# Kernel tuning notes

Measured on AMD Instinct MI355X. Metric: run time of the kernel, lower is better.

The kernel has to match this reference:

```python
import jax, jax.numpy as jnp
import numpy as np

N, E, NFEAT, H = 100000, 1600000, 128, 128
NLAYER = 3


def setup_inputs() -> dict:
    key = jax.random.key(0)
    ks = jax.random.split(key, 20)
    s = 0.05
    return {
        "features": jax.random.normal(ks[0], (N, NFEAT), jnp.float32),
        "edge_index": jax.random.randint(ks[1], (2, E), 0, N, jnp.int32),
        "edge_weight": jax.random.uniform(ks[2], (E,), jnp.float32),
        "w1": jax.random.normal(ks[3], (H, NFEAT), jnp.float32) * s,
        "b1": jnp.zeros((H,), jnp.float32),
        "gin_w1": jax.random.normal(ks[4], (NLAYER, H, H), jnp.float32) * s,
        "gin_b1": jnp.zeros((NLAYER, H), jnp.float32),
        "gin_w2": jax.random.normal(ks[5], (NLAYER, H, H), jnp.float32) * s,
        "gin_b2": jnp.zeros((NLAYER, H), jnp.float32),
        "gru_wih": jax.random.normal(ks[6], (NLAYER, 3 * H, H), jnp.float32) * s,
        "gru_whh": jax.random.normal(ks[7], (NLAYER, 3 * H, H), jnp.float32) * s,
        "gru_bih": jnp.zeros((NLAYER, 3 * H), jnp.float32),
        "gru_bhh": jnp.zeros((NLAYER, 3 * H), jnp.float32),
        "head_w1": jax.random.normal(ks[8], (NLAYER, H, H), jnp.float32) * s,
        "head_b1": jnp.zeros((NLAYER, H), jnp.float32),
        "head_w2_0": jax.random.normal(ks[9], (2, H), jnp.float32) * s,
        "head_b2_0": jnp.zeros((2,), jnp.float32),
        "head_w2_1": jax.random.normal(ks[10], (6, H), jnp.float32) * s,
        "head_b2_1": jnp.zeros((6,), jnp.float32),
        "head_w2_2": jax.random.normal(ks[11], (21, H), jnp.float32) * s,
        "head_b2_2": jnp.zeros((21,), jnp.float32),
    }


def _gru_cell(x, h, wih, whh, bih, bhh):
    # torch.nn.GRUCell semantics
    gi = x @ wih.T + bih           # [N, 3H]
    gh = h @ whh.T + bhh           # [N, 3H]
    ir, iz, inn = jnp.split(gi, 3, axis=1)
    hr, hz, hn = jnp.split(gh, 3, axis=1)
    r = jax.nn.sigmoid(ir + hr)
    z = jax.nn.sigmoid(iz + hz)
    n = jnp.tanh(inn + r * hn)
    return (1.0 - z) * n + z * h


def reference(features, edge_index, edge_weight, w1, b1,
              gin_w1, gin_b1, gin_w2, gin_b2,
              gru_wih, gru_whh, gru_bih, gru_bhh,
              head_w1, head_b1,
              head_w2_0, head_b2_0, head_w2_1, head_b2_1, head_w2_2, head_b2_2):
    n_nodes = features.shape[0]
    dst, src = edge_index[0], edge_index[1]  # spmm: out[dst] += w * x[src]
    head_w2 = [head_w2_0, head_w2_1, head_w2_2]
    head_b2 = [head_b2_0, head_b2_1, head_b2_2]

    x = jax.nn.relu(features @ w1.T + b1)  # mlp1 + ReLU
    layer_info = x
    outputs, _outputs = [], []
    for i in range(NLAYER):
        agg = jax.ops.segment_sum(edge_weight[:, None] * x[src], dst,
                                  num_segments=n_nodes)
        h = _gru_cell(agg, layer_info, gru_wih[i], gru_whh[i],
                      gru_bih[i], gru_bhh[i])
        # GinMlp: Linear -> ReLU -> Linear, then outer ReLU
        x = jax.nn.relu(h @ gin_w1[i].T + gin_b1[i]) @ gin_w2[i].T + gin_b2[i]
        x = jax.nn.relu(x)
        # custom layer-norm variant
        x = x / jnp.sqrt(1.0 + jnp.sum(x * x, axis=1, keepdims=True))
        # prediction head for this layer (mlpPos = [0,1,2])
        tmp = jax.nn.relu(x @ head_w1[i].T + head_b1[i]) @ head_w2[i].T + head_b2[i]
        outputs.append(jax.nn.log_softmax(tmp, axis=1))
        _outputs.append(jax.nn.softmax(tmp, axis=1))
        layer_info = x
    return tuple(outputs) + tuple(_outputs)
```

## Files before the change

### kernel.cpp

```cpp
#include <hip/hip_runtime.h>
#include <cstdint>
#include <cstddef>


typedef short  v8s __attribute__((ext_vector_type(8)));
typedef float  v4f __attribute__((ext_vector_type(4)));

#define BUCKET_CAP 4096

static __device__ __forceinline__ float bf2f(uint16_t u) {
  return __uint_as_float(((uint32_t)u) << 16);
}
static __device__ __forceinline__ uint16_t f2b(float f) {
  uint32_t x = __float_as_uint(f);
  return (uint16_t)((x + 0x7FFFu + ((x >> 16) & 1u)) >> 16);
}
static __device__ __forceinline__ float sigmoidf_(float v) {
  return 1.f / (1.f + __expf(-v));
}
static __device__ __forceinline__ float tanhf_(float v) {
  return 1.f - 2.f / (__expf(2.f * v) + 1.f);
}

__global__ void k_detect(const uint32_t* __restrict__ u, int* __restrict__ flag) {
  int lane = threadIdx.x;
  uint32_t low = u[lane] & 0xFFFFu;
  uint32_t e = (low >> 7) & 0xFFu;
  bool pass = (e == 0) || (e >= 110 && e <= 141);
  unsigned long long b = __ballot(pass);
  if (lane == 0) *flag = (__popcll(b) >= 32) ? 1 : 0;
}

struct CvtDesc {
  const void* src[18];
  int off[19];
};

__global__ void k_cvtw(CvtDesc c, float* __restrict__ wbase,
                       uint16_t* __restrict__ wb16,
                       const int* __restrict__ flag, int total) {
  int gid = blockIdx.x * 256 + threadIdx.x;
  if (gid >= total) return;
  int t = 0;
#pragma unroll
  for (int i = 1; i < 18; i++)
    if (gid >= c.off[i]) t = i;
  int local = gid - c.off[t];
  float v;
  if (*flag) v = bf2f(((const uint16_t*)c.src[t])[local]);
  else       v = ((const float*)c.src[t])[local];
  wbase[gid] = v;
  wb16[gid] = f2b(v);
}

__global__ void k_cvt_feat(const void* __restrict__ src, uint16_t* __restrict__ dst,
                           int n, const int* __restrict__ flag) {
  int i = blockIdx.x * 256 + threadIdx.x;
  if (i >= n) return;
  if (*flag) dst[i] = ((const uint16_t*)src)[i];
  else       dst[i] = f2b(((const float*)src)[i]);
}

__global__ void k_zero_i(int* __restrict__ p, int n) {
  int i = blockIdx.x * 256 + threadIdx.x;
  if (i < n) p[i] = 0;
}

__global__ void k_zero_f(float* __restrict__ p, int n) {
  int i = blockIdx.x * 256 + threadIdx.x;
  if (i < n) p[i] = 0.f;
}

__global__ void k_pack_mm(const uint16_t* __restrict__ src, uint16_t* __restrict__ dst,
                          int nmat) {
  int id = blockIdx.x * 256 + threadIdx.x;
  if (id >= nmat * 2048) return;
  int mat = id >> 11;
  int rem = id & 2047;
  int blk = rem >> 6, lane = rem & 63;
  int kc = blk >> 3, t = blk & 7;
  int n0 = lane & 15, quad = lane >> 4;
  const uint16_t* s = src + (size_t)mat * 16384 + (size_t)(t * 16 + n0) * 128 + kc * 32 + quad * 8;
  uint16_t* d = dst + (size_t)id * 8;
  *reinterpret_cast<v8s*>(d) = *reinterpret_cast<const v8s*>(s);
}

__global__ void k_pack_gru(const uint16_t* __restrict__ wih, const uint16_t* __restrict__ whh,
                           uint16_t* __restrict__ dst, int nlayer) {
  int id = blockIdx.x * 256 + threadIdx.x;
  if (id >= nlayer * 192 * 64) return;
  int lane = id & 63;
  int blk = (id >> 6) % 192;
  int layer = (id >> 6) / 192;
  int g = blk % 3;
  int mat = (blk / 3) % 2;
  int u = (blk / 6) % 2;
  int w = (blk / 12) % 4;
  int kc = blk / 48;
  int n0 = lane & 15, quad = lane >> 4;
  const uint16_t* base = (mat == 0 ? wih : whh) + (size_t)layer * 384 * 128;
  const uint16_t* s = base + (size_t)(g * 128 + w * 32 + u * 16 + n0) * 128 + kc * 32 + quad * 8;
  uint16_t* d = dst + ((size_t)layer * 192 + blk) * 512 + (size_t)lane * 8;
  *reinterpret_cast<v8s*>(d) = *reinterpret_cast<const v8s*>(s);
}

__global__ void k_part(const int* __restrict__ dst, const int* __restrict__ src,
                       const void* __restrict__ w, int* __restrict__ gcur,
                       uint2* __restrict__ ep0, const int* __restrict__ flag,
                       int E, int NB) {
  __shared__ int hist[1024];
  __shared__ int lbase[1024];
  int t = threadIdx.x;
  int CH = (E + gridDim.x - 1) / gridDim.x;
  int e0 = blockIdx.x * CH;
  int e1 = e0 + CH;
  if (e1 > E) e1 = E;
  for (int b = t; b < NB; b += 256) hist[b] = 0;
  __syncthreads();
  for (int e = e0 + t; e < e1; e += 256)
    atomicAdd(&hist[dst[e] >> 7], 1);
  __syncthreads();
  for (int b = t; b < NB; b += 256) {
    int c = hist[b];
    lbase[b] = c ? atomicAdd(&gcur[b], c) : 0;
    hist[b] = 0;
  }
  __syncthreads();
  bool bf = (*flag) != 0;
  for (int e = e0 + t; e < e1; e += 256) {
    int d = dst[e];
    int b = d >> 7;
    int pos = lbase[b] + atomicAdd(&hist[b], 1);
    if (pos >= BUCKET_CAP) pos = BUCKET_CAP - 1;
    float wv = bf ? bf2f(((const uint16_t*)w)[e]) : ((const float*)w)[e];
    ep0[(size_t)b * BUCKET_CAP + pos] =
        make_uint2((uint32_t)src[e] | (((uint32_t)d & 127u) << 25),
                   __float_as_uint(wv));
  }
}

__global__ void k_bprefix(const int* __restrict__ gcur, int* __restrict__ bbase,
                          int nbuckets) {
  __shared__ int red[256];
  int t = threadIdx.x;
  int chunk = (nbuckets + 255) >> 8;
  int beg = t * chunk;
  int end = beg + chunk;
  if (end > nbuckets) end = nbuckets;
  int s = 0;
  for (int b = beg; b < end; b++) {
    int c = gcur[b];
    if (c > BUCKET_CAP) c = BUCKET_CAP;
    bbase[b] = c;
    s += c;
  }
  red[t] = s;
  __syncthreads();
  for (int off = 1; off < 256; off <<= 1) {
    int u = (t >= off) ? red[t - off] : 0;
    __syncthreads();
    red[t] += u;
    __syncthreads();
  }
  int run = red[t] - s;
  for (int b = beg; b < end; b++) {
    int tot = bbase[b];
    bbase[b] = run;
    run += tot;
  }
}

__global__ void k_build(const uint2* __restrict__ ep0, const int* __restrict__ gcur,
                        const int* __restrict__ bbase, int* __restrict__ rowptr,
                        uint2* __restrict__ ep, int n, int nbuckets) {
  __shared__ int lcnt[128];
  __shared__ int lsc[128];
  int b = blockIdx.x, t = threadIdx.x;
  int cnt = gcur[b];
  if (cnt > BUCKET_CAP) cnt = BUCKET_CAP;
  if (t < 128) lcnt[t] = 0;
  __syncthreads();

  const uint2* sp = ep0 + (size_t)b * BUCKET_CAP;
  for (int p = t; p < cnt; p += 256)
    atomicAdd(&lcnt[sp[p].x >> 25], 1);
  __syncthreads();

  if (t < 128) lsc[t] = lcnt[t];
  __syncthreads();
  for (int off = 1; off < 128; off <<= 1) {
    int v = 0;
    if (t < 128 && t >= off) v = lsc[t - off];
    __syncthreads();
    if (t < 128) lsc[t] += v;
    __syncthreads();
  }

  int base = bbase[b];
  if (t < 128) {
    int excl = lsc[t] - lcnt[t];
    int node = b * 128 + t;
    if (node < n) rowptr[node] = base + excl;
    lcnt[t] = base + excl;
  }
  if (b == nbuckets - 1 && t == 0) rowptr[n] = base + lsc[127];
  __syncthreads();

  for (int p = t; p < cnt; p += 256) {
    uint2 v = sp[p];
    int pos = atomicAdd(&lcnt[v.x >> 25], 1);
    ep[pos] = make_uint2(v.x & 0x01FFFFFFu, v.y);
  }
}

__global__ void k_spmm(const uint16_t* __restrict__ x, const int* __restrict__ rowptr,
                       const uint2* __restrict__ ep, uint16_t* __restrict__ agg, int n) {
  int node = blockIdx.x * 4 + (threadIdx.x >> 6);
  int lane = threadIdx.x & 63;
  if (node >= n) return;
  int p0 = rowptr[node], p1 = rowptr[node + 1];
  float a0 = 0.f, a1 = 0.f;
  const uint16_t* xc = x + (size_t)lane * 2;
  int p = p0;
  for (; p + 7 < p1; p += 8) {
    uint2 e0 = ep[p], e1 = ep[p + 1], e2 = ep[p + 2], e3 = ep[p + 3];
    uint2 e4 = ep[p + 4], e5 = ep[p + 5], e6 = ep[p + 6], e7 = ep[p + 7];
    uint32_t u0 = *reinterpret_cast<const uint32_t*>(xc + (size_t)e0.x * 128);
    uint32_t u1 = *reinterpret_cast<const uint32_t*>(xc + (size_t)e1.x * 128);
    uint32_t u2 = *reinterpret_cast<const uint32_t*>(xc + (size_t)e2.x * 128);
    uint32_t u3 = *reinterpret_cast<const uint32_t*>(xc + (size_t)e3.x * 128);
    uint32_t u4 = *reinterpret_cast<const uint32_t*>(xc + (size_t)e4.x * 128);
    uint32_t u5 = *reinterpret_cast<const uint32_t*>(xc + (size_t)e5.x * 128);
    uint32_t u6 = *reinterpret_cast<const uint32_t*>(xc + (size_t)e6.x * 128);
    uint32_t u7 = *reinterpret_cast<const uint32_t*>(xc + (size_t)e7.x * 128);
    float w0 = __uint_as_float(e0.y), w1 = __uint_as_float(e1.y);
    float w2 = __uint_as_float(e2.y), w3 = __uint_as_float(e3.y);
    float w4 = __uint_as_float(e4.y), w5 = __uint_as_float(e5.y);
    float w6 = __uint_as_float(e6.y), w7 = __uint_as_float(e7.y);
    a0 = fmaf(w0, bf2f((uint16_t)u0), a0);
    a1 = fmaf(w0, bf2f((uint16_t)(u0 >> 16)), a1);
    a0 = fmaf(w1, bf2f((uint16_t)u1), a0);
    a1 = fmaf(w1, bf2f((uint16_t)(u1 >> 16)), a1);
    a0 = fmaf(w2, bf2f((uint16_t)u2), a0);
    a1 = fmaf(w2, bf2f((uint16_t)(u2 >> 16)), a1);
    a0 = fmaf(w3, bf2f((uint16_t)u3), a0);
    a1 = fmaf(w3, bf2f((uint16_t)(u3 >> 16)), a1);
    a0 = fmaf(w4, bf2f((uint16_t)u4), a0);
    a1 = fmaf(w4, bf2f((uint16_t)(u4 >> 16)), a1);
    a0 = fmaf(w5, bf2f((uint16_t)u5), a0);
    a1 = fmaf(w5, bf2f((uint16_t)(u5 >> 16)), a1);
    a0 = fmaf(w6, bf2f((uint16_t)u6), a0);
    a1 = fmaf(w6, bf2f((uint16_t)(u6 >> 16)), a1);
    a0 = fmaf(w7, bf2f((uint16_t)u7), a0);
    a1 = fmaf(w7, bf2f((uint16_t)(u7 >> 16)), a1);
  }
  for (; p + 1 < p1; p += 2) {
    uint2 e0 = ep[p], e1 = ep[p + 1];
    uint32_t u0 = *reinterpret_cast<const uint32_t*>(xc + (size_t)e0.x * 128);
    uint32_t u1 = *reinterpret_cast<const uint32_t*>(xc + (size_t)e1.x * 128);
    float w0 = __uint_as_float(e0.y), w1 = __uint_as_float(e1.y);
    a0 = fmaf(w0, bf2f((uint16_t)u0), a0);
    a1 = fmaf(w0, bf2f((uint16_t)(u0 >> 16)), a1);
    a0 = fmaf(w1, bf2f((uint16_t)u1), a0);
    a1 = fmaf(w1, bf2f((uint16_t)(u1 >> 16)), a1);
  }
  for (; p < p1; p++) {
    uint2 e0 = ep[p];
    float w0 = __uint_as_float(e0.y);
    uint32_t u0 = *reinterpret_cast<const uint32_t*>(xc + (size_t)e0.x * 128);
    a0 = fmaf(w0, bf2f((uint16_t)u0), a0);
    a1 = fmaf(w0, bf2f((uint16_t)(u0 >> 16)), a1);
  }
  uint32_t packed = (uint32_t)f2b(a0) | ((uint32_t)f2b(a1) << 16);
  *reinterpret_cast<uint32_t*>(agg + (size_t)node * 128 + lane * 2) = packed;
}

template <int EPI>
__launch_bounds__(256)
__global__ void k_mm(const uint16_t* __restrict__ A, const uint16_t* __restrict__ Wrp,
                     const float* __restrict__ bias, uint16_t* __restrict__ C,
                     int nrows) {
  int wave = threadIdx.x >> 6, lane = threadIdx.x & 63;
  int n0 = lane & 15, quad = lane >> 4;
  int m0 = (blockIdx.x * 4 + wave) * 32;
  int r0 = m0 + n0, r1 = m0 + 16 + n0;
  bool ok0 = r0 < nrows, ok1 = r1 < nrows;
  const v8s z8 = {0, 0, 0, 0, 0, 0, 0, 0};

  v4f acc[2][8];
#pragma unroll
  for (int rt = 0; rt < 2; rt++)
#pragma unroll
    for (int t = 0; t < 8; t++) acc[rt][t] = {0.f, 0.f, 0.f, 0.f};

  const uint16_t* ap0 = A + (size_t)r0 * 128 + quad * 8;
  const uint16_t* ap1 = A + (size_t)r1 * 128 + quad * 8;
#pragma unroll
  for (int kc = 0; kc < 4; kc++) {
    v8s a0 = ok0 ? *reinterpret_cast<const v8s*>(ap0 + kc * 32) : z8;
    v8s a1 = ok1 ? *reinterpret_cast<const v8s*>(ap1 + kc * 32) : z8;
    const uint16_t* wp = Wrp + (size_t)kc * 4096 + (size_t)lane * 8;
#pragma unroll
    for (int t = 0; t < 8; t++) {
      v8s bf = *reinterpret_cast<const v8s*>(wp + t * 512);
      acc[0][t] = __builtin_amdgcn_mfma_f32_16x16x32_bf16(a0, bf, acc[0][t], 0, 0, 0);
      acc[1][t] = __builtin_amdgcn_mfma_f32_16x16x32_bf16(a1, bf, acc[1][t], 0, 0, 0);
    }
  }

#pragma unroll
  for (int rt = 0; rt < 2; rt++) {
    int mb = m0 + rt * 16;
    float vv[8][4];
#pragma unroll
    for (int t = 0; t < 8; t++) {
      float b = bias[t * 16 + n0];
#pragma unroll
      for (int r = 0; r < 4; r++) vv[t][r] = fmaxf(acc[rt][t][r] + b, 0.f);
    }
    if (EPI == 2) {
#pragma unroll
      for (int r = 0; r < 4; r++) {
        float ss = 0.f;
#pragma unroll
        for (int t = 0; t < 8; t++) ss = fmaf(vv[t][r], vv[t][r], ss);
        ss += __shfl_xor(ss, 1);
        ss += __shfl_xor(ss, 2);
        ss += __shfl_xor(ss, 4);
        ss += __shfl_xor(ss, 8);
        float sc = rsqrtf(1.f + ss);
#pragma unroll
        for (int t = 0; t < 8; t++) vv[t][r] *= sc;
      }
    }
#pragma unroll
    for (int r = 0; r < 4; r++) {
      int row = mb + quad * 4 + r;
      if (row >= nrows) continue;
#pragma unroll
      for (int t = 0; t < 8; t++)
        C[(size_t)row * 128 + t * 16 + n0] = f2b(vv[t][r]);
    }
  }
}

template <int C>
__launch_bounds__(256)
__global__ void k_mm12h(const uint16_t* __restrict__ A,
                        const uint16_t* __restrict__ W1rp, const float* __restrict__ b1,
                        const uint16_t* __restrict__ W2rp, const float* __restrict__ b2,
                        const uint16_t* __restrict__ Whrp, const float* __restrict__ bh,
                        const float* __restrict__ w2, const float* __restrict__ b2h,
                        uint16_t* __restrict__ xbout,
                        float* __restrict__ out_log, float* __restrict__ out_soft,
                        int nrows) {
  __shared__ uint16_t hl[128][136];
  int wave = threadIdx.x >> 6, lane = threadIdx.x & 63;
  int n0 = lane & 15, quad = lane >> 4;
  int m0 = (blockIdx.x * 4 + wave) * 32;
  int r0 = m0 + n0, r1 = m0 + 16 + n0;
  bool ok0 = r0 < nrows, ok1 = r1 < nrows;
  const v8s z8 = {0, 0, 0, 0, 0, 0, 0, 0};

  v4f acc[2][8];
#pragma unroll
  for (int rt = 0; rt < 2; rt++)
#pragma unroll
    for (int t = 0; t < 8; t++) acc[rt][t] = {0.f, 0.f, 0.f, 0.f};

  const uint16_t* ap0 = A + (size_t)r0 * 128 + quad * 8;
  const uint16_t* ap1 = A + (size_t)r1 * 128 + quad * 8;
#pragma unroll
  for (int kc = 0; kc < 4; kc++) {
    v8s a0 = ok0 ? *reinterpret_cast<const v8s*>(ap0 + kc * 32) : z8;
    v8s a1 = ok1 ? *reinterpret_cast<const v8s*>(ap1 + kc * 32) : z8;
    const uint16_t* wp = W1rp + (size_t)kc * 4096 + (size_t)lane * 8;
#pragma unroll
    for (int t = 0; t < 8; t++) {
      v8s bf = *reinterpret_cast<const v8s*>(wp + t * 512);
      acc[0][t] = __builtin_amdgcn_mfma_f32_16x16x32_bf16(a0, bf, acc[0][t], 0, 0, 0);
      acc[1][t] = __builtin_amdgcn_mfma_f32_16x16x32_bf16(a1, bf, acc[1][t], 0, 0, 0);
    }
  }
#pragma unroll
  for (int rt = 0; rt < 2; rt++) {
#pragma unroll
    for (int t = 0; t < 8; t++) {
      float b = b1[t * 16 + n0];
#pragma unroll
      for (int r = 0; r < 4; r++) {
        int rl = wave * 32 + rt * 16 + quad * 4 + r;
        hl[rl][t * 16 + n0] = f2b(fmaxf(acc[rt][t][r] + b, 0.f));
      }
    }
  }
  __syncthreads();

  v4f acc2[2][8];
#pragma unroll
  for (int rt = 0; rt < 2; rt++)
#pragma unroll
    for (int t = 0; t < 8; t++) acc2[rt][t] = {0.f, 0.f, 0.f, 0.f};
#pragma unroll
  for (int kc = 0; kc < 4; kc++) {
    v8s a0 = *reinterpret_cast<const v8s*>(&hl[wave * 32 + n0][kc * 32 + quad * 8]);
    v8s a1 = *reinterpret_cast<const v8s*>(&hl[wave * 32 + 16 + n0][kc * 32 + quad * 8]);
    const uint16_t* wp = W2rp + (size_t)kc * 4096 + (size_t)lane * 8;
#pragma unroll
    for (int t = 0; t < 8; t++) {
      v8s bf = *reinterpret_cast<const v8s*>(wp + t * 512);
      acc2[0][t] = __builtin_amdgcn_mfma_f32_16x16x32_bf16(a0, bf, acc2[0][t], 0, 0, 0);
      acc2[1][t] = __builtin_amdgcn_mfma_f32_16x16x32_bf16(a1, bf, acc2[1][t], 0, 0, 0);
    }
  }
  __syncthreads();
#pragma unroll
  for (int rt = 0; rt < 2; rt++) {
    int mb = m0 + rt * 16;
    float vv[8][4];
#pragma unroll
    for (int t = 0; t < 8; t++) {
      float b = b2[t * 16 + n0];
#pragma unroll
      for (int r = 0; r < 4; r++) vv[t][r] = fmaxf(acc2[rt][t][r] + b, 0.f);
    }
#pragma unroll
    for (int r = 0; r < 4; r++) {
      float ss = 0.f;
#pragma unroll
      for (int t = 0; t < 8; t++) ss = fmaf(vv[t][r], vv[t][r], ss);
      ss += __shfl_xor(ss, 1);
      ss += __shfl_xor(ss, 2);
      ss += __shfl_xor(ss, 4);
      ss += __shfl_xor(ss, 8);
      float sc = rsqrtf(1.f + ss);
#pragma unroll
      for (int t = 0; t < 8; t++) vv[t][r] *= sc;
    }
#pragma unroll
    for (int r = 0; r < 4; r++) {
      int row = mb + quad * 4 + r;
      int rl = wave * 32 + rt * 16 + quad * 4 + r;
#pragma unroll
      for (int t = 0; t < 8; t++) {
        uint16_t hv = f2b(vv[t][r]);
        hl[rl][t * 16 + n0] = hv;
        if (row < nrows) xbout[(size_t)row * 128 + t * 16 + n0] = hv;
      }
    }
  }
  __syncthreads();

  v4f acc3[2][8];
#pragma unroll
  for (int rt = 0; rt < 2; rt++)
#pragma unroll
    for (int t = 0; t < 8; t++) acc3[rt][t] = {0.f, 0.f, 0.f, 0.f};
#pragma unroll
  for (int kc = 0; kc < 4; kc++) {
    v8s a0 = *reinterpret_cast<const v8s*>(&hl[wave * 32 + n0][kc * 32 + quad * 8]);
    v8s a1 = *reinterpret_cast<const v8s*>(&hl[wave * 32 + 16 + n0][kc * 32 + quad * 8]);
    const uint16_t* wp = Whrp + (size_t)kc * 4096 + (size_t)lane * 8;
#pragma unroll
    for (int t = 0; t < 8; t++) {
      v8s bf = *reinterpret_cast<const v8s*>(wp + t * 512);
      acc3[0][t] = __builtin_amdgcn_mfma_f32_16x16x32_bf16(a0, bf, acc3[0][t], 0, 0, 0);
      acc3[1][t] = __builtin_amdgcn_mfma_f32_16x16x32_bf16(a1, bf, acc3[1][t], 0, 0, 0);
    }
  }
  __syncthreads();
#pragma unroll
  for (int rt = 0; rt < 2; rt++) {
#pragma unroll
    for (int t = 0; t < 8; t++) {
      float b = bh[t * 16 + n0];
#pragma unroll
      for (int r = 0; r < 4; r++) {
        int rl = wave * 32 + rt * 16 + quad * 4 + r;
        hl[rl][t * 16 + n0] = f2b(fmaxf(acc3[rt][t][r] + b, 0.f));
      }
    }
  }
  __syncthreads();

  int tid = threadIdx.x;
  if (tid < 128) {
    int node = blockIdx.x * 128 + tid;
    if (node < nrows) {
      float lg[C];
#pragma unroll
      for (int c = 0; c < C; c++) lg[c] = b2h[c];
      for (int k = 0; k < 64; k++) {
        uint32_t u = *reinterpret_cast<const uint32_t*>(&hl[tid][2 * k]);
        float x0 = bf2f((uint16_t)u);
        float x1 = bf2f((uint16_t)(u >> 16));
#pragma unroll
        for (int c = 0; c < C; c++) lg[c] = fmaf(x0, w2[c * 128 + 2 * k], lg[c]);
#pragma unroll
        for (int c = 0; c < C; c++) lg[c] = fmaf(x1, w2[c * 128 + 2 * k + 1], lg[c]);
      }
      float m = lg[0];
#pragma unroll
      for (int c = 1; c < C; c++) m = fmaxf(m, lg[c]);
      float sum = 0.f;
      float e[C];
#pragma unroll
      for (int c = 0; c < C; c++) { e[c] = __expf(lg[c] - m); sum += e[c]; }
      float ls = __logf(sum);
      float inv = 1.f / sum;
#pragma unroll
      for (int c = 0; c < C; c++) {
        out_log[(size_t)node * C + c] = lg[c] - m - ls;
        out_soft[(size_t)node * C + c] = e[c] * inv;
      }
    }
  }
}

__launch_bounds__(512, 2)
__global__ void k_gru8(const uint16_t* __restrict__ agg, const uint16_t* __restrict__ xb,
                       const uint16_t* __restrict__ Wrp,
                       const float* __restrict__ bih, const float* __restrict__ bhh,
                       uint16_t* __restrict__ hb, int n, int ntiles) {
  int wave = threadIdx.x >> 6, lane = threadIdx.x & 63;
  int n0 = lane & 15, quad = lane >> 4;
  int s = wave >> 1, u = wave & 1;
  const v8s z8 = {0, 0, 0, 0, 0, 0, 0, 0};

  v8s wf[24];
#pragma unroll
  for (int kc = 0; kc < 4; kc++)
#pragma unroll
    for (int mat = 0; mat < 2; mat++)
#pragma unroll
      for (int g = 0; g < 3; g++)
        wf[kc * 6 + mat * 3 + g] = *reinterpret_cast<const v8s*>(
            Wrp + (size_t)((kc * 4 + s) * 12 + (u * 2 + mat) * 3 + g) * 512 +
            (size_t)lane * 8);

  int col = wave * 16 + n0;
  float bir = bih[col], biz = bih[128 + col], bin = bih[256 + col];
  float bhr = bhh[col], bhz = bhh[128 + col], bhn = bhh[256 + col];

  for (int tt = blockIdx.x; tt < ntiles; tt += gridDim.x) {
    int m0 = tt * 32;
    int r0 = m0 + n0, r1 = m0 + 16 + n0;
    bool ok0 = r0 < n, ok1 = r1 < n;

    v4f accI[2][3], accH[2][3];
#pragma unroll
    for (int rt = 0; rt < 2; rt++)
#pragma unroll
      for (int g = 0; g < 3; g++) {
        accI[rt][g] = {0.f, 0.f, 0.f, 0.f};
        accH[rt][g] = {0.f, 0.f, 0.f, 0.f};
      }

    const uint16_t* ap0 = agg + (size_t)r0 * 128 + quad * 8;
    const uint16_t* ap1 = agg + (size_t)r1 * 128 + quad * 8;
    const uint16_t* xp0 = xb + (size_t)r0 * 128 + quad * 8;
    const uint16_t* xp1 = xb + (size_t)r1 * 128 + quad * 8;
#pragma unroll
    for (int kc = 0; kc < 4; kc++) {
      v8s a0 = ok0 ? *reinterpret_cast<const v8s*>(ap0 + kc * 32) : z8;
      v8s a1 = ok1 ? *reinterpret_cast<const v8s*>(ap1 + kc * 32) : z8;
      v8s x0 = ok0 ? *reinterpret_cast<const v8s*>(xp0 + kc * 32) : z8;
      v8s x1 = ok1 ? *reinterpret_cast<const v8s*>(xp1 + kc * 32) : z8;
#pragma unroll
      for (int g = 0; g < 3; g++) {
        accI[0][g] = __builtin_amdgcn_mfma_f32_16x16x32_bf16(a0, wf[kc * 6 + g], accI[0][g], 0, 0, 0);
        accI[1][g] = __builtin_amdgcn_mfma_f32_16x16x32_bf16(a1, wf[kc * 6 + g], accI[1][g], 0, 0, 0);
        accH[0][g] = __builtin_amdgcn_mfma_f32_16x16x32_bf16(x0, wf[kc * 6 + 3 + g], accH[0][g], 0, 0, 0);
        accH[1][g] = __builtin_amdgcn_mfma_f32_16x16x32_bf16(x1, wf[kc * 6 + 3 + g], accH[1][g], 0, 0, 0);
      }
    }

#pragma unroll
    for (int rt = 0; rt < 2; rt++) {
#pragma unroll
      for (int r = 0; r < 4; r++) {
        int row = m0 + rt * 16 + quad * 4 + r;
        if (row < n) {
          float ir = accI[rt][0][r] + bir;
          float iz = accI[rt][1][r] + biz;
          float in_ = accI[rt][2][r] + bin;
          float hr = accH[rt][0][r] + bhr;
          float hz = accH[rt][1][r] + bhz;
          float hn = accH[rt][2][r] + bhn;
          float rr = sigmoidf_(ir + hr);
          float zz = sigmoidf_(iz + hz);
          float nn = tanhf_(fmaf(rr, hn, in_));
          float xv = bf2f(xb[(size_t)row * 128 + col]);
          hb[(size_t)row * 128 + col] = f2b(fmaf(zz, xv - nn, nn));
        }
      }
    }
  }
}

extern "C" void kernel_launch(void* const* d_in, const int* in_sizes, int n_in,
                              void* d_out, int out_size, void* d_ws, size_t ws_size,
                              hipStream_t stream) {
  const int N = in_sizes[0] / 128;
  const int E = in_sizes[2];
  const int NB = (N + 127) >> 7;

  static const int wn[18] = {16384, 128, 49152, 384, 49152, 384,
                             147456, 147456, 1152, 1152, 49152, 384,
                             256, 2, 768, 6, 2688, 21};
  CvtDesc cd;
  int off = 0;
  for (int i = 0; i < 18; i++) {
    cd.src[i] = d_in[3 + i];
    cd.off[i] = off;
    off += wn[i];
  }
  cd.off[18] = off;
  const int wtotal = off;

  char* p = (char*)d_ws;
  size_t used = 0;
  auto alloc = [&](size_t bytes) -> char* {
    char* r = p;
    size_t b = (bytes + 255) & ~(size_t)255;
    p += b;
    used += b;
    return r;
  };
  int*      flag    = (int*)alloc(256);
  float*    wbase   = (float*)alloc((size_t)wtotal * 4);
  uint16_t* wb16    = (uint16_t*)alloc((size_t)wtotal * 2);
  uint16_t* mmrp    = (uint16_t*)alloc((size_t)10 * 16384 * 2);
  uint16_t* grurp   = (uint16_t*)alloc((size_t)3 * 192 * 512 * 2);
  uint16_t* xb      = (uint16_t*)alloc((size_t)N * 128 * 2);
  uint16_t* aggb    = (uint16_t*)alloc((size_t)N * 128 * 2);
  uint16_t* hb      = (uint16_t*)alloc((size_t)N * 128 * 2);
  int*      rowptr  = (int*)alloc((size_t)(N + 1) * 4);
  int*      gcur    = (int*)alloc((size_t)NB * 4);
  int*      bbase   = (int*)alloc((size_t)(NB + 1) * 4);
  uint2*    ep0     = (uint2*)alloc((size_t)NB * BUCKET_CAP * 8);
  uint2*    epack   = (uint2*)alloc((size_t)E * 8);

  float* out = (float*)d_out;
  float* outlog[3]  = {out, out + 2 * (size_t)N, out + 8 * (size_t)N};
  float* outsoft[3] = {out + 29 * (size_t)N, out + 31 * (size_t)N, out + 37 * (size_t)N};

  if (used > ws_size) {
    k_zero_f<<<(out_size + 255) / 256, 256, 0, stream>>>(out, out_size);
    return;
  }

  float* b1f   = wbase + cd.off[1];
  float* ginb1 = wbase + cd.off[3];
  float* ginb2 = wbase + cd.off[5];
  float* bih   = wbase + cd.off[8];
  float* bhh   = wbase + cd.off[9];
  float* hb1   = wbase + cd.off[11];
  float* hw2_0 = wbase + cd.off[12];
  float* hb2_0 = wbase + cd.off[13];
  float* hw2_1 = wbase + cd.off[14];
  float* hb2_1 = wbase + cd.off[15];
  float* hw2_2 = wbase + cd.off[16];
  float* hb2_2 = wbase + cd.off[17];

  uint16_t* w1b   = wb16 + cd.off[0];
  uint16_t* ginw1b= wb16 + cd.off[2];
  uint16_t* ginw2b= wb16 + cd.off[4];
  uint16_t* wihb  = wb16 + cd.off[6];
  uint16_t* whhb  = wb16 + cd.off[7];
  uint16_t* hw1b  = wb16 + cd.off[10];

  uint16_t* w1rp    = mmrp;
  uint16_t* ginw1rp = mmrp + (size_t)1 * 16384;
  uint16_t* ginw2rp = mmrp + (size_t)4 * 16384;
  uint16_t* hw1rp   = mmrp + (size_t)7 * 16384;

  const int* dst = (const int*)d_in[1];
  const int* src = (const int*)d_in[1] + E;

  k_detect<<<1, 64, 0, stream>>>((const uint32_t*)d_in[0], flag);
  k_cvtw<<<(wtotal + 255) / 256, 256, 0, stream>>>(cd, wbase, wb16, flag, wtotal);
  k_cvt_feat<<<((size_t)N * 128 + 255) / 256, 256, 0, stream>>>(d_in[0], aggb,
                                                                N * 128, flag);
  k_pack_mm<<<(1 * 2048 + 255) / 256, 256, 0, stream>>>(w1b, w1rp, 1);
  k_pack_mm<<<(3 * 2048 + 255) / 256, 256, 0, stream>>>(ginw1b, ginw1rp, 3);
  k_pack_mm<<<(3 * 2048 + 255) / 256, 256, 0, stream>>>(ginw2b, ginw2rp, 3);
  k_pack_mm<<<(3 * 2048 + 255) / 256, 256, 0, stream>>>(hw1b, hw1rp, 3);
  k_pack_gru<<<(3 * 192 * 64 + 255) / 256, 256, 0, stream>>>(wihb, whhb, grurp, 3);

  k_zero_i<<<(NB + 255) / 256, 256, 0, stream>>>(gcur, NB);
  k_part<<<256, 256, 0, stream>>>(dst, src, d_in[2], gcur, ep0, flag, E, NB);
  k_bprefix<<<1, 256, 0, stream>>>(gcur, bbase, NB);
  k_build<<<NB, 256, 0, stream>>>(ep0, gcur, bbase, rowptr, epack, N, NB);

  int mmrb = (N + 127) / 128;
  int spb  = (N + 3) / 4;
  int ntiles32 = (N + 31) / 32;

  k_mm<1><<<mmrb, 256, 0, stream>>>(aggb, w1rp, b1f, xb, N);

  for (int i = 0; i < 3; i++) {
    k_spmm<<<spb, 256, 0, stream>>>(xb, rowptr, epack, aggb, N);
    k_gru8<<<256, 512, 0, stream>>>(aggb, xb, grurp + (size_t)i * 192 * 512,
                                    bih + i * 384, bhh + i * 384, hb, N, ntiles32);
    if (i == 0)
      k_mm12h<2><<<mmrb, 256, 0, stream>>>(hb, ginw1rp + (size_t)i * 16384,
                                           ginb1 + i * 128,
                                           ginw2rp + (size_t)i * 16384,
                                           ginb2 + i * 128,
                                           hw1rp + (size_t)i * 16384, hb1 + i * 128,
                                           hw2_0, hb2_0, xb,
                                           outlog[0], outsoft[0], N);
    else if (i == 1)
      k_mm12h<6><<<mmrb, 256, 0, stream>>>(hb, ginw1rp + (size_t)i * 16384,
                                           ginb1 + i * 128,
                                           ginw2rp + (size_t)i * 16384,
                                           ginb2 + i * 128,
                                           hw1rp + (size_t)i * 16384, hb1 + i * 128,
                                           hw2_1, hb2_1, xb,
                                           outlog[1], outsoft[1], N);
    else
      k_mm12h<21><<<mmrb, 256, 0, stream>>>(hb, ginw1rp + (size_t)i * 16384,
                                            ginb1 + i * 128,
                                            ginw2rp + (size_t)i * 16384,
                                            ginb2 + i * 128,
                                            hw1rp + (size_t)i * 16384, hb1 + i * 128,
                                            hw2_2, hb2_2, xb,
                                            outlog[2], outsoft[2], N);
  }
}
```

Before: 814.0 us.

## Halve mm12h row tile and split head output across four threads per row

The fused GIN-MLP/head kernel now handles 64 rows per block (16 per wave) instead of 128, which halves the LDS tile and accumulator registers and doubles the block count. The final small head projection changes from 128 threads each doing a full 128-long dot product to all 256 threads, four per row, each covering a quarter of K and combined with xor shuffles. This is meant to raise occupancy and remove the serial tail where half the block sat idle. In exchange, each weight fragment is reused across fewer rows, so weight loads per row double.

Result: slower. 869.2 us (+6.8%).

```diff
diff --git a/kernel.cpp b/kernel.cpp
--- a/kernel.cpp
+++ b/kernel.cpp
@@ -354,75 +354,61 @@
                         uint16_t* __restrict__ xbout,
                         float* __restrict__ out_log, float* __restrict__ out_soft,
                         int nrows) {
-  __shared__ uint16_t hl[128][136];
+  __shared__ uint16_t hl[64][136];
   int wave = threadIdx.x >> 6, lane = threadIdx.x & 63;
   int n0 = lane & 15, quad = lane >> 4;
-  int m0 = (blockIdx.x * 4 + wave) * 32;
-  int r0 = m0 + n0, r1 = m0 + 16 + n0;
-  bool ok0 = r0 < nrows, ok1 = r1 < nrows;
+  int m0 = blockIdx.x * 64 + wave * 16;
+  int r0 = m0 + n0;
+  bool ok0 = r0 < nrows;
   const v8s z8 = {0, 0, 0, 0, 0, 0, 0, 0};
 
-  v4f acc[2][8];
-#pragma unroll
-  for (int rt = 0; rt < 2; rt++)
-#pragma unroll
-    for (int t = 0; t < 8; t++) acc[rt][t] = {0.f, 0.f, 0.f, 0.f};
+  v4f acc[8];
+#pragma unroll
+  for (int t = 0; t < 8; t++) acc[t] = {0.f, 0.f, 0.f, 0.f};
 
   const uint16_t* ap0 = A + (size_t)r0 * 128 + quad * 8;
-  const uint16_t* ap1 = A + (size_t)r1 * 128 + quad * 8;
 #pragma unroll
   for (int kc = 0; kc < 4; kc++) {
     v8s a0 = ok0 ? *reinterpret_cast<const v8s*>(ap0 + kc * 32) : z8;
-    v8s a1 = ok1 ? *reinterpret_cast<const v8s*>(ap1 + kc * 32) : z8;
     const uint16_t* wp = W1rp + (size_t)kc * 4096 + (size_t)lane * 8;
 #pragma unroll
     for (int t = 0; t < 8; t++) {
       v8s bf = *reinterpret_cast<const v8s*>(wp + t * 512);
-      acc[0][t] = __builtin_amdgcn_mfma_f32_16x16x32_bf16(a0, bf, acc[0][t], 0, 0, 0);
-      acc[1][t] = __builtin_amdgcn_mfma_f32_16x16x32_bf16(a1, bf, acc[1][t], 0, 0, 0);
-    }
-  }
-#pragma unroll
-  for (int rt = 0; rt < 2; rt++) {
-#pragma unroll
-    for (int t = 0; t < 8; t++) {
-      float b = b1[t * 16 + n0];
-#pragma unroll
-      for (int r = 0; r < 4; r++) {
-        int rl = wave * 32 + rt * 16 + quad * 4 + r;
-        hl[rl][t * 16 + n0] = f2b(fmaxf(acc[rt][t][r] + b, 0.f));
-      }
-    }
-  }
-  __syncthreads();
-
-  v4f acc2[2][8];
-#pragma unroll
-  for (int rt = 0; rt < 2; rt++)
-#pragma unroll
-    for (int t = 0; t < 8; t++) acc2[rt][t] = {0.f, 0.f, 0.f, 0.f};
+      acc[t] = __builtin_amdgcn_mfma_f32_16x16x32_bf16(a0, bf, acc[t], 0, 0, 0);
+    }
+  }
+#pragma unroll
+  for (int t = 0; t < 8; t++) {
+    float b = b1[t * 16 + n0];
+#pragma unroll
+    for (int r = 0; r < 4; r++) {
+      int rl = wave * 16 + quad * 4 + r;
+      hl[rl][t * 16 + n0] = f2b(fmaxf(acc[t][r] + b, 0.f));
+    }
+  }
+  __syncthreads();
+
+  v4f acc2[8];
+#pragma unroll
+  for (int t = 0; t < 8; t++) acc2[t] = {0.f, 0.f, 0.f, 0.f};
 #pragma unroll
   for (int kc = 0; kc < 4; kc++) {
-    v8s a0 = *reinterpret_cast<const v8s*>(&hl[wave * 32 + n0][kc * 32 + quad * 8]);
-    v8s a1 = *reinterpret_cast<const v8s*>(&hl[wave * 32 + 16 + n0][kc * 32 + quad * 8]);
+    v8s a0 = *reinterpret_cast<const v8s*>(&hl[wave * 16 + n0][kc * 32 + quad * 8]);
     const uint16_t* wp = W2rp + (size_t)kc * 4096 + (size_t)lane * 8;
 #pragma unroll
     for (int t = 0; t < 8; t++) {
       v8s bf = *reinterpret_cast<const v8s*>(wp + t * 512);
-      acc2[0][t] = __builtin_amdgcn_mfma_f32_16x16x32_bf16(a0, bf, acc2[0][t], 0, 0, 0);
-      acc2[1][t] = __builtin_amdgcn_mfma_f32_16x16x32_bf16(a1, bf, acc2[1][t], 0, 0, 0);
-    }
-  }
-  __syncthreads();
-#pragma unroll
-  for (int rt = 0; rt < 2; rt++) {
-    int mb = m0 + rt * 16;
+      acc2[t] = __builtin_amdgcn_mfma_f32_16x16x32_bf16(a0, bf, acc2[t], 0, 0, 0);
+    }
+  }
+  __syncthreads();
+  {
     float vv[8][4];
 #pragma unroll
     for (int t = 0; t < 8; t++) {
       float b = b2[t * 16 + n0];
 #pragma unroll
-      for (int r = 0; r < 4; r++) vv[t][r] = fmaxf(acc2[rt][t][r] + b, 0.f);
+      for (int r = 0; r < 4; r++) vv[t][r] = fmaxf(acc2[t][r] + b, 0.f);
     }
 #pragma unroll
     for (int r = 0; r < 4; r++) {
@@ -439,8 +425,8 @@
     }
 #pragma unroll
     for (int r = 0; r < 4; r++) {
-      int row = mb + quad * 4 + r;
-      int rl = wave * 32 + rt * 16 + quad * 4 + r;
+      int row = m0 + quad * 4 + r;
+      int rl = wave * 16 + quad * 4 + r;
 #pragma unroll
       for (int t = 0; t < 8; t++) {
         uint16_t hv = f2b(vv[t][r]);
@@ -451,54 +437,58 @@
   }
   __syncthreads();
 
-  v4f acc3[2][8];
-#pragma unroll
-  for (int rt = 0; rt < 2; rt++)
-#pragma unroll
-    for (int t = 0; t < 8; t++) acc3[rt][t] = {0.f, 0.f, 0.f, 0.f};
+  v4f acc3[8];
+#pragma unroll
+  for (int t = 0; t < 8; t++) acc3[t] = {0.f, 0.f, 0.f, 0.f};
 #pragma unroll
   for (int kc = 0; kc < 4; kc++) {
-    v8s a0 = *reinterpret_cast<const v8s*>(&hl[wave * 32 + n0][kc * 32 + quad * 8]);
-    v8s a1 = *reinterpret_cast<const v8s*>(&hl[wave * 32 + 16 + n0][kc * 32 + quad * 8]);
+    v8s a0 = *reinterpret_cast<const v8s*>(&hl[wave * 16 + n0][kc * 32 + quad * 8]);
     const uint16_t* wp = Whrp + (size_t)kc * 4096 + (size_t)lane * 8;
 #pragma unroll
     for (int t = 0; t < 8; t++) {
       v8s bf = *reinterpret_cast<const v8s*>(wp + t * 512);
-      acc3[0][t] = __builtin_amdgcn_mfma_f32_16x16x32_bf16(a0, bf, acc3[0][t], 0, 0, 0);
-      acc3[1][t] = __builtin_amdgcn_mfma_f32_16x16x32_bf16(a1, bf, acc3[1][t], 0, 0, 0);
-    }
-  }
-  __syncthreads();
-#pragma unroll
-  for (int rt = 0; rt < 2; rt++) {
-#pragma unroll
-    for (int t = 0; t < 8; t++) {
-      float b = bh[t * 16 + n0];
-#pragma unroll
-      for (int r = 0; r < 4; r++) {
-        int rl = wave * 32 + rt * 16 + quad * 4 + r;
-        hl[rl][t * 16 + n0] = f2b(fmaxf(acc3[rt][t][r] + b, 0.f));
-      }
-    }
-  }
-  __syncthreads();
-
-  int tid = threadIdx.x;
-  if (tid < 128) {
-    int node = blockIdx.x * 128 + tid;
-    if (node < nrows) {
-      float lg[C];
-#pragma unroll
-      for (int c = 0; c < C; c++) lg[c] = b2h[c];
-      for (int k = 0; k < 64; k++) {
-        uint32_t u = *reinterpret_cast<const uint32_t*>(&hl[tid][2 * k]);
-        float x0 = bf2f((uint16_t)u);
-        float x1 = bf2f((uint16_t)(u >> 16));
-#pragma unroll
-        for (int c = 0; c < C; c++) lg[c] = fmaf(x0, w2[c * 128 + 2 * k], lg[c]);
-#pragma unroll
-        for (int c = 0; c < C; c++) lg[c] = fmaf(x1, w2[c * 128 + 2 * k + 1], lg[c]);
-      }
+      acc3[t] = __builtin_amdgcn_mfma_f32_16x16x32_bf16(a0, bf, acc3[t], 0, 0, 0);
+    }
+  }
+  __syncthreads();
+#pragma unroll
+  for (int t = 0; t < 8; t++) {
+    float b = bh[t * 16 + n0];
+#pragma unroll
+    for (int r = 0; r < 4; r++) {
+      int rl = wave * 16 + quad * 4 + r;
+      hl[rl][t * 16 + n0] = f2b(fmaxf(acc3[t][r] + b, 0.f));
+    }
+  }
+  __syncthreads();
+
+  {
+    int row = threadIdx.x >> 2;
+    int s = threadIdx.x & 3;
+    int node = blockIdx.x * 64 + row;
+    float lg[C];
+#pragma unroll
+    for (int c = 0; c < C; c++) lg[c] = 0.f;
+    const uint32_t* hr = reinterpret_cast<const uint32_t*>(&hl[row][0]);
+#pragma unroll
+    for (int j = 0; j < 16; j++) {
+      uint32_t u = hr[j * 4 + s];
+      float x0 = bf2f((uint16_t)u);
+      float x1 = bf2f((uint16_t)(u >> 16));
+      int k0 = 2 * (j * 4 + s);
+#pragma unroll
+      for (int c = 0; c < C; c++) lg[c] = fmaf(x0, w2[c * 128 + k0], lg[c]);
+#pragma unroll
+      for (int c = 0; c < C; c++) lg[c] = fmaf(x1, w2[c * 128 + k0 + 1], lg[c]);
+    }
+#pragma unroll
+    for (int c = 0; c < C; c++) {
+      lg[c] += __shfl_xor(lg[c], 1);
+      lg[c] += __shfl_xor(lg[c], 2);
+    }
+    if (s == 0 && node < nrows) {
+#pragma unroll
+      for (int c = 0; c < C; c++) lg[c] += b2h[c];
       float m = lg[0];
 #pragma unroll
       for (int c = 1; c < C; c++) m = fmaxf(m, lg[c]);
@@ -694,6 +684,7 @@
   k_build<<<NB, 256, 0, stream>>>(ep0, gcur, bbase, rowptr, epack, N, NB);
 
   int mmrb = (N + 127) / 128;
+  int mmhb = (N + 63) / 64;
   int spb  = (N + 3) / 4;
   int ntiles32 = (N + 31) / 32;
 
@@ -704,7 +695,7 @@
     k_gru8<<<256, 512, 0, stream>>>(aggb, xb, grurp + (size_t)i * 192 * 512,
                                     bih + i * 384, bhh + i * 384, hb, N, ntiles32);
     if (i == 0)
-      k_mm12h<2><<<mmrb, 256, 0, stream>>>(hb, ginw1rp + (size_t)i * 16384,
+      k_mm12h<2><<<mmhb, 256, 0, stream>>>(hb, ginw1rp + (size_t)i * 16384,
                                            ginb1 + i * 128,
                                            ginw2rp + (size_t)i * 16384,
                                            ginb2 + i * 128,
@@ -712,7 +703,7 @@
                                            hw2_0, hb2_0, xb,
                                            outlog[0], outsoft[0], N);
     else if (i == 1)
-      k_mm12h<6><<<mmrb, 256, 0, stream>>>(hb, ginw1rp + (size_t)i * 16384,
+      k_mm12h<6><<<mmhb, 256, 0, stream>>>(hb, ginw1rp + (size_t)i * 16384,
                                            ginb1 + i * 128,
                                            ginw2rp + (size_t)i * 16384,
                                            ginb2 + i * 128,
@@ -720,7 +711,7 @@
                                            hw2_1, hb2_1, xb,
                                            outlog[1], outsoft[1], N);
     else
-      k_mm12h<21><<<mmrb, 256, 0, stream>>>(hb, ginw1rp + (size_t)i * 16384,
+      k_mm12h<21><<<mmhb, 256, 0, stream>>>(hb, ginw1rp + (size_t)i * 16384,
                                             ginb1 + i * 128,
                                             ginw2rp + (size_t)i * 16384,
                                             ginb2 + i * 128,
```

## Split fused GIN/head kernel into persistent kernels with LDS-resident weights

Applied to the files above, without the earlier changes.

Replaces the fused three-matmul-plus-head kernel with two persistent kernels. The first GIN linear runs in a grid-stride kernel that keeps each wave's weight fragment in registers, and writes its activations to the reused agg buffer. The second GIN linear and the head run in a kernel that stages both weight matrices and the small head weights in LDS. Each wave works independently on 32-row tiles with no block barriers, and the head dot products are split across lane pairs. This adds an extra global round trip of the intermediate activations in exchange for cutting repeated global weight fetches and syncs.

Result: slower. 839.3 us (+3.1%).

```diff
diff --git a/kernel.cpp b/kernel.cpp
--- a/kernel.cpp
+++ b/kernel.cpp
@@ -344,174 +344,201 @@
   }
 }
 
-template <int C>
-__launch_bounds__(256)
-__global__ void k_mm12h(const uint16_t* __restrict__ A,
-                        const uint16_t* __restrict__ W1rp, const float* __restrict__ b1,
-                        const uint16_t* __restrict__ W2rp, const float* __restrict__ b2,
-                        const uint16_t* __restrict__ Whrp, const float* __restrict__ bh,
-                        const float* __restrict__ w2, const float* __restrict__ b2h,
-                        uint16_t* __restrict__ xbout,
-                        float* __restrict__ out_log, float* __restrict__ out_soft,
-                        int nrows) {
-  __shared__ uint16_t hl[128][136];
+__launch_bounds__(512, 2)
+__global__ void k_gin1(const uint16_t* __restrict__ hb, const uint16_t* __restrict__ W1rp,
+                       const float* __restrict__ b1, uint16_t* __restrict__ tmp,
+                       int n, int ntiles) {
   int wave = threadIdx.x >> 6, lane = threadIdx.x & 63;
   int n0 = lane & 15, quad = lane >> 4;
-  int m0 = (blockIdx.x * 4 + wave) * 32;
-  int r0 = m0 + n0, r1 = m0 + 16 + n0;
-  bool ok0 = r0 < nrows, ok1 = r1 < nrows;
   const v8s z8 = {0, 0, 0, 0, 0, 0, 0, 0};
 
-  v4f acc[2][8];
-#pragma unroll
-  for (int rt = 0; rt < 2; rt++)
-#pragma unroll
-    for (int t = 0; t < 8; t++) acc[rt][t] = {0.f, 0.f, 0.f, 0.f};
-
-  const uint16_t* ap0 = A + (size_t)r0 * 128 + quad * 8;
-  const uint16_t* ap1 = A + (size_t)r1 * 128 + quad * 8;
-#pragma unroll
-  for (int kc = 0; kc < 4; kc++) {
-    v8s a0 = ok0 ? *reinterpret_cast<const v8s*>(ap0 + kc * 32) : z8;
-    v8s a1 = ok1 ? *reinterpret_cast<const v8s*>(ap1 + kc * 32) : z8;
-    const uint16_t* wp = W1rp + (size_t)kc * 4096 + (size_t)lane * 8;
-#pragma unroll
-    for (int t = 0; t < 8; t++) {
-      v8s bf = *reinterpret_cast<const v8s*>(wp + t * 512);
-      acc[0][t] = __builtin_amdgcn_mfma_f32_16x16x32_bf16(a0, bf, acc[0][t], 0, 0, 0);
-      acc[1][t] = __builtin_amdgcn_mfma_f32_16x16x32_bf16(a1, bf, acc[1][t], 0, 0, 0);
-    }
-  }
-#pragma unroll
-  for (int rt = 0; rt < 2; rt++) {
-#pragma unroll
-    for (int t = 0; t < 8; t++) {
-      float b = b1[t * 16 + n0];
+  v8s wf[4];
+#pragma unroll
+  for (int kc = 0; kc < 4; kc++)
+    wf[kc] = *reinterpret_cast<const v8s*>(
+        W1rp + (size_t)(kc * 8 + wave) * 512 + (size_t)lane * 8);
+
+  int col = wave * 16 + n0;
+  float bb = b1[col];
+
+  for (int tt = blockIdx.x; tt < ntiles; tt += gridDim.x) {
+    int m0 = tt * 32;
+    int r0 = m0 + n0, r1 = m0 + 16 + n0;
+    bool ok0 = r0 < n, ok1 = r1 < n;
+    v4f acc0 = {0.f, 0.f, 0.f, 0.f};
+    v4f acc1 = {0.f, 0.f, 0.f, 0.f};
+    const uint16_t* ap0 = hb + (size_t)r0 * 128 + quad * 8;
+    const uint16_t* ap1 = hb + (size_t)r1 * 128 + quad * 8;
+#pragma unroll
+    for (int kc = 0; kc < 4; kc++) {
+      v8s a0 = ok0 ? *reinterpret_cast<const v8s*>(ap0 + kc * 32) : z8;
+      v8s a1 = ok1 ? *reinterpret_cast<const v8s*>(ap1 + kc * 32) : z8;
+      acc0 = __builtin_amdgcn_mfma_f32_16x16x32_bf16(a0, wf[kc], acc0, 0, 0, 0);
+      acc1 = __builtin_amdgcn_mfma_f32_16x16x32_bf16(a1, wf[kc], acc1, 0, 0, 0);
+    }
+#pragma unroll
+    for (int r = 0; r < 4; r++) {
+      int row0 = m0 + quad * 4 + r;
+      int row1 = m0 + 16 + quad * 4 + r;
+      if (row0 < n) tmp[(size_t)row0 * 128 + col] = f2b(fmaxf(acc0[r] + bb, 0.f));
+      if (row1 < n) tmp[(size_t)row1 * 128 + col] = f2b(fmaxf(acc1[r] + bb, 0.f));
+    }
+  }
+}
+
+template <int C>
+__launch_bounds__(512)
+__global__ void k_g2h(const uint16_t* __restrict__ tmp,
+                      const uint16_t* __restrict__ W2rp, const float* __restrict__ b2,
+                      const uint16_t* __restrict__ Whrp, const float* __restrict__ bh,
+                      const float* __restrict__ w2, const float* __restrict__ b2h,
+                      uint16_t* __restrict__ xbout,
+                      float* __restrict__ out_log, float* __restrict__ out_soft,
+                      int n, int ntiles) {
+  __shared__ uint16_t W2l[16384];
+  __shared__ uint16_t Whl[16384];
+  __shared__ float w2l[128 * C];
+  __shared__ uint16_t sc[8][32][136];
+  int tid = threadIdx.x;
+
+  for (int i = tid; i < 2048; i += 512)
+    reinterpret_cast<v8s*>(W2l)[i] = reinterpret_cast<const v8s*>(W2rp)[i];
+  for (int i = tid; i < 2048; i += 512)
+    reinterpret_cast<v8s*>(Whl)[i] = reinterpret_cast<const v8s*>(Whrp)[i];
+  for (int i = tid; i < 128 * C; i += 512) w2l[i] = w2[i];
+  __syncthreads();
+
+  int wave = tid >> 6, lane = tid & 63;
+  int n0 = lane & 15, quad = lane >> 4;
+  const v8s z8 = {0, 0, 0, 0, 0, 0, 0, 0};
+  uint16_t (*scw)[136] = sc[wave];
+
+  for (int tt = blockIdx.x * 8 + wave; tt < ntiles; tt += gridDim.x * 8) {
+    int m0 = tt * 32;
+    int r0 = m0 + n0, r1 = m0 + 16 + n0;
+    bool ok0 = r0 < n, ok1 = r1 < n;
+
+    v4f acc[2][8];
+#pragma unroll
+    for (int rt = 0; rt < 2; rt++)
+#pragma unroll
+      for (int t = 0; t < 8; t++) acc[rt][t] = {0.f, 0.f, 0.f, 0.f};
+    const uint16_t* ap0 = tmp + (size_t)r0 * 128 + quad * 8;
+    const uint16_t* ap1 = tmp + (size_t)r1 * 128 + quad * 8;
+#pragma unroll
+    for (int kc = 0; kc < 4; kc++) {
+      v8s a0 = ok0 ? *reinterpret_cast<const v8s*>(ap0 + kc * 32) : z8;
+      v8s a1 = ok1 ? *reinterpret_cast<const v8s*>(ap1 + kc * 32) : z8;
+#pragma unroll
+      for (int t = 0; t < 8; t++) {
+        v8s bf = *reinterpret_cast<const v8s*>(&W2l[(size_t)(kc * 8 + t) * 512 + (size_t)lane * 8]);
+        acc[0][t] = __builtin_amdgcn_mfma_f32_16x16x32_bf16(a0, bf, acc[0][t], 0, 0, 0);
+        acc[1][t] = __builtin_amdgcn_mfma_f32_16x16x32_bf16(a1, bf, acc[1][t], 0, 0, 0);
+      }
+    }
+
+#pragma unroll
+    for (int rt = 0; rt < 2; rt++) {
+      float vv[8][4];
+#pragma unroll
+      for (int t = 0; t < 8; t++) {
+        float b = b2[t * 16 + n0];
+#pragma unroll
+        for (int r = 0; r < 4; r++) vv[t][r] = fmaxf(acc[rt][t][r] + b, 0.f);
+      }
 #pragma unroll
       for (int r = 0; r < 4; r++) {
-        int rl = wave * 32 + rt * 16 + quad * 4 + r;
-        hl[rl][t * 16 + n0] = f2b(fmaxf(acc[rt][t][r] + b, 0.f));
-      }
-    }
-  }
-  __syncthreads();
-
-  v4f acc2[2][8];
-#pragma unroll
-  for (int rt = 0; rt < 2; rt++)
-#pragma unroll
-    for (int t = 0; t < 8; t++) acc2[rt][t] = {0.f, 0.f, 0.f, 0.f};
-#pragma unroll
-  for (int kc = 0; kc < 4; kc++) {
-    v8s a0 = *reinterpret_cast<const v8s*>(&hl[wave * 32 + n0][kc * 32 + quad * 8]);
-    v8s a1 = *reinterpret_cast<const v8s*>(&hl[wave * 32 + 16 + n0][kc * 32 + quad * 8]);
-    const uint16_t* wp = W2rp + (size_t)kc * 4096 + (size_t)lane * 8;
-#pragma unroll
-    for (int t = 0; t < 8; t++) {
-      v8s bf = *reinterpret_cast<const v8s*>(wp + t * 512);
-      acc2[0][t] = __builtin_amdgcn_mfma_f32_16x16x32_bf16(a0, bf, acc2[0][t], 0, 0, 0);
-      acc2[1][t] = __builtin_amdgcn_mfma_f32_16x16x32_bf16(a1, bf, acc2[1][t], 0, 0, 0);
-    }
-  }
-  __syncthreads();
-#pragma unroll
-  for (int rt = 0; rt < 2; rt++) {
-    int mb = m0 + rt * 16;
-    float vv[8][4];
-#pragma unroll
-    for (int t = 0; t < 8; t++) {
-      float b = b2[t * 16 + n0];
-#pragma unroll
-      for (int r = 0; r < 4; r++) vv[t][r] = fmaxf(acc2[rt][t][r] + b, 0.f);
-    }
-#pragma unroll
-    for (int r = 0; r < 4; r++) {
-      float ss = 0.f;
-#pragma unroll
-      for (int t = 0; t < 8; t++) ss = fmaf(vv[t][r], vv[t][r], ss);
-      ss += __shfl_xor(ss, 1);
-      ss += __shfl_xor(ss, 2);
-      ss += __shfl_xor(ss, 4);
-      ss += __shfl_xor(ss, 8);
-      float sc = rsqrtf(1.f + ss);
-#pragma unroll
-      for (int t = 0; t < 8; t++) vv[t][r] *= sc;
-    }
-#pragma unroll
-    for (int r = 0; r < 4; r++) {
-      int row = mb + quad * 4 + r;
-      int rl = wave * 32 + rt * 16 + quad * 4 + r;
+        float ss = 0.f;
+#pragma unroll
+        for (int t = 0; t < 8; t++) ss = fmaf(vv[t][r], vv[t][r], ss);
+        ss += __shfl_xor(ss, 1);
+        ss += __shfl_xor(ss, 2);
+        ss += __shfl_xor(ss, 4);
+        ss += __shfl_xor(ss, 8);
+        float scn = rsqrtf(1.f + ss);
+#pragma unroll
+        for (int t = 0; t < 8; t++) vv[t][r] *= scn;
+      }
+#pragma unroll
+      for (int r = 0; r < 4; r++) {
+        int rl = rt * 16 + quad * 4 + r;
+        int row = m0 + rl;
+#pragma unroll
+        for (int t = 0; t < 8; t++) {
+          uint16_t hv = f2b(vv[t][r]);
+          scw[rl][t * 16 + n0] = hv;
+          if (row < n) xbout[(size_t)row * 128 + t * 16 + n0] = hv;
+        }
+      }
+    }
+
+    v4f acc3[2][8];
+#pragma unroll
+    for (int rt = 0; rt < 2; rt++)
+#pragma unroll
+      for (int t = 0; t < 8; t++) acc3[rt][t] = {0.f, 0.f, 0.f, 0.f};
+#pragma unroll
+    for (int kc = 0; kc < 4; kc++) {
+      v8s a0 = *reinterpret_cast<const v8s*>(&scw[n0][kc * 32 + quad * 8]);
+      v8s a1 = *reinterpret_cast<const v8s*>(&scw[16 + n0][kc * 32 + quad * 8]);
 #pragma unroll
       for (int t = 0; t < 8; t++) {
-        uint16_t hv = f2b(vv[t][r]);
-        hl[rl][t * 16 + n0] = hv;
-        if (row < nrows) xbout[(size_t)row * 128 + t * 16 + n0] = hv;
-      }
-    }
-  }
-  __syncthreads();
-
-  v4f acc3[2][8];
-#pragma unroll
-  for (int rt = 0; rt < 2; rt++)
-#pragma unroll
-    for (int t = 0; t < 8; t++) acc3[rt][t] = {0.f, 0.f, 0.f, 0.f};
-#pragma unroll
-  for (int kc = 0; kc < 4; kc++) {
-    v8s a0 = *reinterpret_cast<const v8s*>(&hl[wave * 32 + n0][kc * 32 + quad * 8]);
-    v8s a1 = *reinterpret_cast<const v8s*>(&hl[wave * 32 + 16 + n0][kc * 32 + quad * 8]);
-    const uint16_t* wp = Whrp + (size_t)kc * 4096 + (size_t)lane * 8;
-#pragma unroll
-    for (int t = 0; t < 8; t++) {
-      v8s bf = *reinterpret_cast<const v8s*>(wp + t * 512);
-      acc3[0][t] = __builtin_amdgcn_mfma_f32_16x16x32_bf16(a0, bf, acc3[0][t], 0, 0, 0);
-      acc3[1][t] = __builtin_amdgcn_mfma_f32_16x16x32_bf16(a1, bf, acc3[1][t], 0, 0, 0);
-    }
-  }
-  __syncthreads();
-#pragma unroll
-  for (int rt = 0; rt < 2; rt++) {
-#pragma unroll
-    for (int t = 0; t < 8; t++) {
-      float b = bh[t * 16 + n0];
-#pragma unroll
-      for (int r = 0; r < 4; r++) {
-        int rl = wave * 32 + rt * 16 + quad * 4 + r;
-        hl[rl][t * 16 + n0] = f2b(fmaxf(acc3[rt][t][r] + b, 0.f));
-      }
-    }
-  }
-  __syncthreads();
-
-  int tid = threadIdx.x;
-  if (tid < 128) {
-    int node = blockIdx.x * 128 + tid;
-    if (node < nrows) {
+        v8s bf = *reinterpret_cast<const v8s*>(&Whl[(size_t)(kc * 8 + t) * 512 + (size_t)lane * 8]);
+        acc3[0][t] = __builtin_amdgcn_mfma_f32_16x16x32_bf16(a0, bf, acc3[0][t], 0, 0, 0);
+        acc3[1][t] = __builtin_amdgcn_mfma_f32_16x16x32_bf16(a1, bf, acc3[1][t], 0, 0, 0);
+      }
+    }
+#pragma unroll
+    for (int rt = 0; rt < 2; rt++) {
+#pragma unroll
+      for (int t = 0; t < 8; t++) {
+        float b = bh[t * 16 + n0];
+#pragma unroll
+        for (int r = 0; r < 4; r++) {
+          int rl = rt * 16 + quad * 4 + r;
+          scw[rl][t * 16 + n0] = f2b(fmaxf(acc3[rt][t][r] + b, 0.f));
+        }
+      }
+    }
+
+    {
+      int rowl = lane >> 1;
+      int s = lane & 1;
+      int node = m0 + rowl;
       float lg[C];
 #pragma unroll
-      for (int c = 0; c < C; c++) lg[c] = b2h[c];
-      for (int k = 0; k < 64; k++) {
-        uint32_t u = *reinterpret_cast<const uint32_t*>(&hl[tid][2 * k]);
+      for (int c = 0; c < C; c++) lg[c] = 0.f;
+      const uint32_t* hr = reinterpret_cast<const uint32_t*>(&scw[rowl][0]);
+#pragma unroll
+      for (int j = 0; j < 32; j++) {
+        uint32_t u = hr[j * 2 + s];
         float x0 = bf2f((uint16_t)u);
         float x1 = bf2f((uint16_t)(u >> 16));
-#pragma unroll
-        for (int c = 0; c < C; c++) lg[c] = fmaf(x0, w2[c * 128 + 2 * k], lg[c]);
-#pragma unroll
-        for (int c = 0; c < C; c++) lg[c] = fmaf(x1, w2[c * 128 + 2 * k + 1], lg[c]);
-      }
-      float m = lg[0];
-#pragma unroll
-      for (int c = 1; c < C; c++) m = fmaxf(m, lg[c]);
-      float sum = 0.f;
-      float e[C];
-#pragma unroll
-      for (int c = 0; c < C; c++) { e[c] = __expf(lg[c] - m); sum += e[c]; }
-      float ls = __logf(sum);
-      float inv = 1.f / sum;
-#pragma unroll
-      for (int c = 0; c < C; c++) {
-        out_log[(size_t)node * C + c] = lg[c] - m - ls;
-        out_soft[(size_t)node * C + c] = e[c] * inv;
+        int k0 = 2 * (j * 2 + s);
+#pragma unroll
+        for (int c = 0; c < C; c++) lg[c] = fmaf(x0, w2l[c * 128 + k0], lg[c]);
+#pragma unroll
+        for (int c = 0; c < C; c++) lg[c] = fmaf(x1, w2l[c * 128 + k0 + 1], lg[c]);
+      }
+#pragma unroll
+      for (int c = 0; c < C; c++) lg[c] += __shfl_xor(lg[c], 1);
+      if (s == 0 && node < n) {
+#pragma unroll
+        for (int c = 0; c < C; c++) lg[c] += b2h[c];
+        float m = lg[0];
+#pragma unroll
+        for (int c = 1; c < C; c++) m = fmaxf(m, lg[c]);
+        float sum = 0.f;
+        float e[C];
+#pragma unroll
+        for (int c = 0; c < C; c++) { e[c] = __expf(lg[c] - m); sum += e[c]; }
+        float ls = __logf(sum);
+        float inv = 1.f / sum;
+#pragma unroll
+        for (int c = 0; c < C; c++) {
+          out_log[(size_t)node * C + c] = lg[c] - m - ls;
+          out_soft[(size_t)node * C + c] = e[c] * inv;
+        }
       }
     }
   }
@@ -703,29 +730,25 @@
     k_spmm<<<spb, 256, 0, stream>>>(xb, rowptr, epack, aggb, N);
     k_gru8<<<256, 512, 0, stream>>>(aggb, xb, grurp + (size_t)i * 192 * 512,
                                     bih + i * 384, bhh + i * 384, hb, N, ntiles32);
+    k_gin1<<<256, 512, 0, stream>>>(hb, ginw1rp + (size_t)i * 16384,
+                                    ginb1 + i * 128, aggb, N, ntiles32);
     if (i == 0)
-      k_mm12h<2><<<mmrb, 256, 0, stream>>>(hb, ginw1rp + (size_t)i * 16384,
-                                           ginb1 + i * 128,
-                                           ginw2rp + (size_t)i * 16384,
-                                           ginb2 + i * 128,
-                                           hw1rp + (size_t)i * 16384, hb1 + i * 128,
-                                           hw2_0, hb2_0, xb,
-                                           outlog[0], outsoft[0], N);
+      k_g2h<2><<<256, 512, 0, stream>>>(aggb, ginw2rp + (size_t)i * 16384,
+                                        ginb2 + i * 128,
+                                        hw1rp + (size_t)i * 16384, hb1 + i * 128,
+                                        hw2_0, hb2_0, xb,
+                                        outlog[0], outsoft[0], N, ntiles32);
     else if (i == 1)
-      k_mm12h<6><<<mmrb, 256, 0, stream>>>(hb, ginw1rp + (size_t)i * 16384,
-                                           ginb1 + i * 128,
-                                           ginw2rp + (size_t)i * 16384,
-                                           ginb2 + i * 128,
-                                           hw1rp + (size_t)i * 16384, hb1 + i * 128,
-                                           hw2_1, hb2_1, xb,
-                                           outlog[1], outsoft[1], N);
+      k_g2h<6><<<256, 512, 0, stream>>>(aggb, ginw2rp + (size_t)i * 16384,
+                                        ginb2 + i * 128,
+                                        hw1rp + (size_t)i * 16384, hb1 + i * 128,
+                                        hw2_1, hb2_1, xb,
+                                        outlog[1], outsoft[1], N, ntiles32);
     else
-      k_mm12h<21><<<mmrb, 256, 0, stream>>>(hb, ginw1rp + (size_t)i * 16384,
-                                            ginb1 + i * 128,
-                                            ginw2rp + (size_t)i * 16384,
-                                            ginb2 + i * 128,
-                                            hw1rp + (size_t)i * 16384, hb1 + i * 128,
-                                            hw2_2, hb2_2, xb,
-                                            outlog[2], outsoft[2], N);
-  }
-}
+      k_g2h<21><<<256, 512, 0, stream>>>(aggb, ginw2rp + (size_t)i * 16384,
+                                         ginb2 + i * 128,
+                                         hw1rp + (size_t)i * 16384, hb1 + i * 128,
+                                         hw2_2, hb2_2, xb,
+                                         outlog[2], outsoft[2], N, ntiles32);
+  }
+}
```
